# Optimization experiments

Measured on AMD Instinct MI355X. Metric: run time of the kernel, lower is better.

Reference implementation:

```python
import jax, jax.numpy as jnp
import numpy as np

N, E = 100000, 3200000
IN, HID, OUT, ED = 16, 64, 32, 3
BN_EPS = 1e-5


def setup_inputs() -> dict:
    key = jax.random.key(0)
    ks = jax.random.split(key, 40)
    d = {}
    d["x"] = jax.random.normal(ks[0], (N, IN), jnp.float32)
    d["edge_index"] = jax.random.randint(ks[1], (2, E), 0, N, dtype=jnp.int32)
    d["edge_attr"] = jax.random.normal(ks[2], (E, ED), jnp.float32)
    i = [3]
    def p(shape):
        w = jax.random.normal(ks[i[0]], shape, jnp.float32) * 0.05
        i[0] += 1
        return w
    for tag, nd in (("inj1", IN), ("inj2", HID), ("inj3", HID)):
        d[tag + "_w1"] = p((ED, nd)); d[tag + "_b1"] = p((nd,))
        d[tag + "_w2"] = p((nd, nd)); d[tag + "_b2"] = p((nd,))
    for tag, ci, co in (("conv1", IN, HID), ("conv2", HID, HID), ("conv3", HID, OUT)):
        d[tag + "_wl"] = p((ci, co)); d[tag + "_bl"] = p((co,))
        d[tag + "_wr"] = p((ci, co))
    for tag, c in (("bn1", HID), ("bn2", HID), ("bn3", OUT)):
        d[tag + "_w"] = p((c,)); d[tag + "_b"] = p((c,))
    return d


def _inject(x, src, dst, edge_attr, w1, b1, w2, b2):
    # edge MLP: [E, ED] -> [E, node_dim], sigmoid wind gate from column 2
    h = jax.nn.relu(edge_attr @ w1 + b1) @ w2 + b2
    gate = jax.nn.sigmoid(edge_attr[:, 2:3])
    msg = h * gate
    agg = jax.ops.segment_sum(msg, dst, num_segments=x.shape[0])
    return x + agg


def _sage(x, src, dst, wl, bl, wr):
    # PyG SAGEConv (mean aggr): lin_l(mean_{j in N(i)} x_j) + lin_r(x_i)
    n = x.shape[0]
    s = jax.ops.segment_sum(x[src], dst, num_segments=n)
    cnt = jax.ops.segment_sum(jnp.ones((src.shape[0], 1), x.dtype), dst, num_segments=n)
    mean = s / jnp.maximum(cnt, 1.0)
    return mean @ wl + bl + x @ wr


def _bn(x, w, b):
    # eval-mode BatchNorm with running_mean=0, running_var=1
    return x * (w / jnp.sqrt(1.0 + BN_EPS)) + b


def reference(x, edge_index, edge_attr,
              inj1_w1, inj1_b1, inj1_w2, inj1_b2,
              inj2_w1, inj2_b1, inj2_w2, inj2_b2,
              inj3_w1, inj3_b1, inj3_w2, inj3_b2,
              conv1_wl, conv1_bl, conv1_wr,
              conv2_wl, conv2_bl, conv2_wr,
              conv3_wl, conv3_bl, conv3_wr,
              bn1_w, bn1_b, bn2_w, bn2_b, bn3_w, bn3_b):
    src, dst = edge_index[0], edge_index[1]
    h = _inject(x, src, dst, edge_attr, inj1_w1, inj1_b1, inj1_w2, inj1_b2)
    h = jax.nn.relu(_bn(_sage(h, src, dst, conv1_wl, conv1_bl, conv1_wr), bn1_w, bn1_b))
    h = _inject(h, src, dst, edge_attr, inj2_w1, inj2_b1, inj2_w2, inj2_b2)
    h = jax.nn.relu(_bn(_sage(h, src, dst, conv2_wl, conv2_bl, conv2_wr), bn2_w, bn2_b))
    h = _inject(h, src, dst, edge_attr, inj3_w1, inj3_b1, inj3_w2, inj3_b2)
    h = jax.nn.relu(_bn(_sage(h, src, dst, conv3_wl, conv3_bl, conv3_wr), bn3_w, bn3_b))
    return h
```

## Files before the change

kernel.cpp:

```cpp
#include <hip/hip_runtime.h>
#include <math.h>

#define N_NODES 100000
#define N_EDGES 3200000
#define NB 391
#define CHUNK 4096
#define NCHUNK 782
#define HCHUNK 4096
#define NHCHUNK 782
#define CAPB 10240
#define NPW 4
#define NWAVES ((N_NODES + NPW - 1)/NPW)
#define NBLK_INJ ((NWAVES + 3)/4)

constexpr size_t al512(size_t x){ return (x + 511) & ~size_t(511); }
constexpr size_t o_bcnt = 0;
constexpr size_t o_bst  = al512(o_bcnt + 512*4);
constexpr size_t o_gb   = al512(o_bst  + 512*4);
constexpr size_t o_off  = al512(o_gb   + 512*4);
constexpr size_t o_srcp = al512(o_off  + ((size_t)N_NODES+1)*4);
constexpr size_t o_epk  = al512(o_srcp + (size_t)N_EDGES*4);
constexpr size_t o_U1   = al512(o_epk  + (size_t)N_EDGES*16);
constexpr size_t o_U2   = al512(o_U1   + (size_t)N_NODES*16*4);
constexpr size_t o_U3   = o_U2 + (size_t)N_NODES*64*4;
constexpr size_t o_gs   = al512(o_U3   + (size_t)N_NODES*64*4);
constexpr size_t o_h1   = al512(o_gs   + (size_t)N_NODES*4);
constexpr size_t o_m1   = al512(o_h1   + (size_t)N_NODES*16*4);
constexpr size_t o_rec  = o_U2;
constexpr size_t o_h2bf = o_epk;
constexpr size_t o_h3bf = o_epk + (size_t)N_NODES*128;
constexpr size_t o_m2   = o_U2;
constexpr size_t o_y3   = o_U1;
constexpr size_t o_m3p  = o_U2;

#define BN_RSQRT 0.9999950000374997f

__device__ __forceinline__ float4 ld4(const float* p){ return *(const float4*)p; }
__device__ __forceinline__ float fc(const float4& v, int i){ return ((const float*)&v)[i]; }
__device__ __forceinline__ float uf(unsigned u){ return __uint_as_float(u); }

typedef float v2f __attribute__((ext_vector_type(2)));
__device__ __forceinline__ v2f v2mk(float a, float b){ v2f v; v.x=a; v.y=b; return v; }
__device__ __forceinline__ v2f v2sp(float s){ v2f v; v.x=s; v.y=s; return v; }
__device__ __forceinline__ v2f v2fma(v2f a, v2f b, v2f c){ return __builtin_elementwise_fma(a,b,c); }
__device__ __forceinline__ v2f v2max0(v2f a){ return __builtin_elementwise_max(a, v2sp(0.f)); }

__device__ __forceinline__ unsigned f2bf(float x){
    unsigned u = __float_as_uint(x);
    u += 0x7fffu + ((u >> 16) & 1u);
    return u >> 16;
}

__global__ __launch_bounds__(256) void khistBin(const int* __restrict__ dst,
                                                int* __restrict__ binCnt){
    __shared__ int c[NB];
    int t = threadIdx.x;
    for(int i=t; i<NB; i+=256) c[i] = 0;
    __syncthreads();
    long base = (long)blockIdx.x*HCHUNK;
    int nrem = (int)(N_EDGES - base); if(nrem > HCHUNK) nrem = HCHUNK;
    for(int k=t; k<nrem; k+=256)
        atomicAdd(&c[dst[base+k] >> 8], 1);
    __syncthreads();
    for(int i=t; i<NB; i+=256)
        if(c[i]) atomicAdd(&binCnt[i], c[i]);
}

__global__ __launch_bounds__(512) void kscanBin(const int* __restrict__ binCnt,
                                                int* __restrict__ binStart,
                                                int* __restrict__ gbase){
    __shared__ int s[512];
    int t = threadIdx.x;
    int v = (t < NB) ? binCnt[t] : 0;
    s[t] = v; __syncthreads();
    for(int off=1; off<512; off<<=1){
        int a = (t>=off) ? s[t-off] : 0;
        __syncthreads(); s[t] += a; __syncthreads();
    }
    int ex = (t==0) ? 0 : s[t-1];
    if(t < NB){ binStart[t] = ex; gbase[t] = ex; }
    if(t == NB) binStart[NB] = s[NB-1];
}

__global__ __launch_bounds__(256) void kbinA(const int* __restrict__ src,
                                             const int* __restrict__ dst,
                                             const float* __restrict__ ea,
                                             int* __restrict__ gbase,
                                             unsigned* __restrict__ recD){
    __shared__ int cnt[NB], lofs[NB], gst[NB], lcnt[NB];
    __shared__ int sscan[256];
    __shared__ unsigned stage[CHUNK*3];
    __shared__ unsigned short binOf[CHUNK];
    int t = threadIdx.x;
    long e0i = (long)blockIdx.x*CHUNK;
    int nrem = (int)(N_EDGES - e0i); if(nrem > CHUNK) nrem = CHUNK;
    if(nrem <= 0) return;

    for(int b=t; b<NB; b+=256){ cnt[b]=0; lcnt[b]=0; }
    __syncthreads();
    for(int k=t; k<nrem; k+=256)
        atomicAdd(&cnt[dst[e0i+k] >> 8], 1);
    __syncthreads();
    int c0 = (2*t   < NB) ? cnt[2*t]   : 0;
    int c1 = (2*t+1 < NB) ? cnt[2*t+1] : 0;
    sscan[t] = c0 + c1;
    __syncthreads();
    for(int off=1; off<256; off<<=1){
        int v = (t>=off) ? sscan[t-off] : 0;
        __syncthreads(); sscan[t] += v; __syncthreads();
    }
    int base = (t==0) ? 0 : sscan[t-1];
    if(2*t   < NB) lofs[2*t]   = base;
    if(2*t+1 < NB) lofs[2*t+1] = base + c0;
    for(int b=t; b<NB; b+=256){
        int c = cnt[b];
        gst[b] = c ? atomicAdd(&gbase[b], c) : 0;
    }
    __syncthreads();
    for(int k=t; k<nrem; k+=256){
        long i = e0i + k;
        int d = dst[i];
        int s = src[i];
        float a0 = ea[i*3+0], a1 = ea[i*3+1], a2 = ea[i*3+2];
        int b = d >> 8;
        int p = lofs[b] + atomicAdd(&lcnt[b], 1);
        stage[3*p+0] = (unsigned)s | ((unsigned)(d & 255) << 17);
        stage[3*p+1] = (f2bf(a1)<<16) | f2bf(a0);
        stage[3*p+2] = __float_as_uint(a2);
        binOf[p] = (unsigned short)b;
    }
    __syncthreads();
    int total3 = nrem*3;
    for(int q=t; q<total3; q+=256){
        int p = q/3;
        int r = q - 3*p;
        int b = binOf[p];
        int g = gst[b] + (p - lofs[b]);
        recD[(size_t)3*g + r] = stage[q];
    }
}

__global__ __launch_bounds__(512) void kbinB(const unsigned* __restrict__ recD,
                                             const int* __restrict__ binStart,
                                             int* __restrict__ offs,
                                             int* __restrict__ srcp,
                                             float4* __restrict__ epk){
    __shared__ int pfx[257], lcnt[256];
    __shared__ int sscan[256];
    __shared__ unsigned short perm[CAPB];
    __shared__ unsigned char  nibOf[CAPB];
    int t = threadIdx.x;
    int b = blockIdx.x;
    int n0 = b*256;
    int nn = N_NODES - n0; if(nn > 256) nn = 256;
    int base = binStart[b];
    int m    = binStart[b+1] - base;
    for(int i=t; i<256; i+=512) lcnt[i] = 0;
    __syncthreads();
    for(int p=t; p<m; p+=512){
        unsigned w0 = recD[(size_t)3*(base+p)];
        int nib = (int)((w0 >> 17) & 255u);
        if(p < CAPB) nibOf[p] = (unsigned char)nib;
        atomicAdd(&lcnt[nib], 1);
    }
    __syncthreads();
    if(t < 256) sscan[t] = lcnt[t];
    __syncthreads();
    if(t < 256){
        for(int off=1; off<256; off<<=1){
            int v = (t>=off) ? sscan[t-off] : 0;
            __syncthreads(); sscan[t] += v; __syncthreads();
        }
        pfx[t+1] = sscan[t];
        if(t==0) pfx[0] = 0;
    } else {
        for(int off=1; off<256; off<<=1){ __syncthreads(); __syncthreads(); }
    }
    __syncthreads();
    for(int i=t; i<=nn; i+=512) offs[n0+i] = base + pfx[i];
    for(int i=t; i<256; i+=512) lcnt[i] = 0;
    __syncthreads();
    for(int p=t; p<m; p+=512){
        int nib = nibOf[p];
        int slot = pfx[nib] + atomicAdd(&lcnt[nib], 1);
        perm[slot] = (unsigned short)p;
    }
    __syncthreads();
    for(int s=t; s<m; s+=512){
        size_t q = (size_t)3*(base + (int)perm[s]);
        unsigned w0 = recD[q], w1 = recD[q+1], w2 = recD[q+2];
        float e2 = uf(w2);
        float gate = __builtin_amdgcn_rcpf(1.f + __expf(-e2));
        srcp[base+s] = (int)(w0 & 0x1FFFFu);
        epk [base+s] = make_float4(uf(w1<<16), uf(w1 & 0xffff0000u), e2, gate);
    }
}

#define ACC2(r) { \
    float h1_ = fmaf((r).z,wc1, fmaf((r).y,wb1, fmaf((r).x,wa1, bb1))); \
    a1 = fmaf(fmaxf(h1_,0.f), (r).w, a1); \
    v2f h2_ = v2fma(v2sp((r).z), wc2, v2fma(v2sp((r).y), wb2, v2fma(v2sp((r).x), wa2, bv2))); \
    a2 = v2fma(v2max0(h2_), v2sp((r).w), a2); \
    v2f h3_ = v2fma(v2sp((r).z), wc3, v2fma(v2sp((r).y), wb3, v2fma(v2sp((r).x), wa3, bv3))); \
    a3 = v2fma(v2max0(h3_), v2sp((r).w), a3); \
    g += (r).w; }

__global__ __launch_bounds__(256, 4) void kinject(const float4* __restrict__ epk, const int* __restrict__ offs,
                        const float* __restrict__ w11, const float* __restrict__ b11,
                        const float* __restrict__ w12, const float* __restrict__ b12,
                        const float* __restrict__ w13, const float* __restrict__ b13,
                        float* __restrict__ U1, float* __restrict__ U2,
                        float* __restrict__ U3, float* __restrict__ gsum){
    int wid = (blockIdx.x*256 + threadIdx.x) >> 6;
    int n0 = wid * NPW;
    if(n0 >= N_NODES) return;
    int n1 = n0 + NPW; if(n1 > N_NODES) n1 = N_NODES;
    int lane = threadIdx.x & 63;
    int half = lane >> 5, j = lane & 31, j16 = lane & 15;
    float wa1=w11[j16], wb1=w11[16+j16], wc1=w11[32+j16], bb1=b11[j16];
    v2f wa2=v2mk(w12[j],     w12[32+j]);
    v2f wb2=v2mk(w12[64+j],  w12[96+j]);
    v2f wc2=v2mk(w12[128+j], w12[160+j]);
    v2f bv2=v2mk(b12[j],     b12[32+j]);
    v2f wa3=v2mk(w13[j],     w13[32+j]);
    v2f wb3=v2mk(w13[64+j],  w13[96+j]);
    v2f wc3=v2mk(w13[128+j], w13[160+j]);
    v2f bv3=v2mk(b13[j],     b13[32+j]);

    int beg = offs[n0];
    for(int node=n0; node<n1; ++node){
        int end = offs[node+1];
        float a1=0.f, g=0.f;
        v2f a2=v2sp(0.f), a3=v2sp(0.f);
        int e = beg;
        int efull8 = beg + ((end - beg) & ~7);
        for(; e < efull8; e+=8){
            float4 r0 = epk[e + half];
            float4 r1 = epk[e + 2 + half];
            float4 r2 = epk[e + 4 + half];
            float4 r3 = epk[e + 6 + half];
            ACC2(r0);
            ACC2(r1);
            ACC2(r2);
            ACC2(r3);
        }
        for(; e < end; e+=4){
            int ee0 = e + half, ee1 = e + 2 + half;
            float4 r0 = (ee0 < end) ? epk[ee0] : make_float4(0.f,0.f,0.f,0.f);
            float4 r1 = (ee1 < end) ? epk[ee1] : make_float4(0.f,0.f,0.f,0.f);
            ACC2(r0);
            ACC2(r1);
        }
        a2.x += __shfl_xor(a2.x, 32); a2.y += __shfl_xor(a2.y, 32);
        a3.x += __shfl_xor(a3.x, 32); a3.y += __shfl_xor(a3.y, 32);
        a1   += __shfl_xor(a1, 16);   a1   += __shfl_xor(a1, 32);
        g    += __shfl_xor(g, 32);
        float v2_ = half ? a2.y : a2.x;
        float v3_ = half ? a3.y : a3.x;
        int col = j + 32*half;
        U2[(size_t)node*64 + col] = v2_;
        U3[(size_t)node*64 + col] = v3_;
        if(lane < 16) U1[node*16 + j16] = a1;
        if(lane == 0) gsum[node] = g;
        beg = end;
    }
}

__global__ void kgather16(const float* __restrict__ h, const int* __restrict__ srcp,
                          const int* __restrict__ offs, float* __restrict__ m){
    int gid = blockIdx.x*blockDim.x + threadIdx.x;
    int node = gid >> 6;
    if(node >= N_NODES) return;
    int lane = threadIdx.x & 63;
    int q = lane >> 4, d = lane & 15;
    int beg = offs[node], end = offs[node+1];
    float acc = 0.f;
    int e = beg + q;
    for(; e + 4 < end; e += 8){
        int s0 = srcp[e], s1 = srcp[e+4];
        float v0 = h[(size_t)s0*16 + d];
        float v1 = h[(size_t)s1*16 + d];
        acc += v0 + v1;
    }
    if(e < end) acc += h[(size_t)srcp[e]*16 + d];
    acc += __shfl_down(acc, 32);
    acc += __shfl_down(acc, 16);
    if(lane < 16){
        float c = fmaxf((float)(end-beg), 1.f);
        m[node*16 + lane] = acc / c;
    }
}

__global__ void kgather64bf(const unsigned* __restrict__ hbf, const int* __restrict__ srcp,
                            const int* __restrict__ offs, float* __restrict__ m){
    int gid = blockIdx.x*blockDim.x + threadIdx.x;
    int node = gid >> 6;
    if(node >= N_NODES) return;
    int lane = threadIdx.x & 63;
    int q = lane >> 4, j = lane & 15;
    int beg = offs[node], end = offs[node+1];
    float4 acc = make_float4(0.f,0.f,0.f,0.f);
    int e = beg;
    int efull16 = beg + ((end - beg) & ~15);
    for(; e < efull16; e+=16){
        int s0 = srcp[e + q],     s1 = srcp[e + 4 + q];
        int s2 = srcp[e + 8 + q], s3 = srcp[e + 12 + q];
        uint2 w0 = *(const uint2*)(hbf + (size_t)s0*32 + 2*j);
        uint2 w1 = *(const uint2*)(hbf + (size_t)s1*32 + 2*j);
        uint2 w2 = *(const uint2*)(hbf + (size_t)s2*32 + 2*j);
        uint2 w3 = *(const uint2*)(hbf + (size_t)s3*32 + 2*j);
        acc.x += uf(w0.x<<16); acc.y += uf(w0.x & 0xffff0000u);
        acc.z += uf(w0.y<<16); acc.w += uf(w0.y & 0xffff0000u);
        acc.x += uf(w1.x<<16); acc.y += uf(w1.x & 0xffff0000u);
        acc.z += uf(w1.y<<16); acc.w += uf(w1.y & 0xffff0000u);
        acc.x += uf(w2.x<<16); acc.y += uf(w2.x & 0xffff0000u);
        acc.z += uf(w2.y<<16); acc.w += uf(w2.y & 0xffff0000u);
        acc.x += uf(w3.x<<16); acc.y += uf(w3.x & 0xffff0000u);
        acc.z += uf(w3.y<<16); acc.w += uf(w3.y & 0xffff0000u);
    }
    int efull8 = beg + ((end - beg) & ~7);
    for(; e < efull8; e+=8){
        int s0 = srcp[e + q], s1 = srcp[e + 4 + q];
        uint2 w0 = *(const uint2*)(hbf + (size_t)s0*32 + 2*j);
        uint2 w1 = *(const uint2*)(hbf + (size_t)s1*32 + 2*j);
        acc.x += uf(w0.x<<16); acc.y += uf(w0.x & 0xffff0000u);
        acc.z += uf(w0.y<<16); acc.w += uf(w0.y & 0xffff0000u);
        acc.x += uf(w1.x<<16); acc.y += uf(w1.x & 0xffff0000u);
        acc.z += uf(w1.y<<16); acc.w += uf(w1.y & 0xffff0000u);
    }
    for(; e < end; e+=4){
        int ee = e + q;
        if(ee < end){
            int s = srcp[ee];
            uint2 w = *(const uint2*)(hbf + (size_t)s*32 + 2*j);
            acc.x += uf(w.x<<16); acc.y += uf(w.x & 0xffff0000u);
            acc.z += uf(w.y<<16); acc.w += uf(w.y & 0xffff0000u);
        }
    }
    acc.x += __shfl_xor(acc.x,16); acc.x += __shfl_xor(acc.x,32);
    acc.y += __shfl_xor(acc.y,16); acc.y += __shfl_xor(acc.y,32);
    acc.z += __shfl_xor(acc.z,16); acc.z += __shfl_xor(acc.z,32);
    acc.w += __shfl_xor(acc.w,16); acc.w += __shfl_xor(acc.w,32);
    if(lane < 16){
        float inv = 1.f / fmaxf((float)(end-beg), 1.f);
        float4 o; o.x=acc.x*inv; o.y=acc.y*inv; o.z=acc.z*inv; o.w=acc.w*inv;
        *(float4*)(m + (size_t)node*64 + 4*j) = o;
    }
}

__global__ void kgather32bf(const unsigned* __restrict__ y3, const int* __restrict__ srcp,
                            const int* __restrict__ offs, float* __restrict__ m){
    int gid = blockIdx.x*blockDim.x + threadIdx.x;
    int node = gid >> 6;
    if(node >= N_NODES) return;
    int lane = threadIdx.x & 63;
    int q = lane >> 4, j = lane & 15;
    int beg = offs[node], end = offs[node+1];
    float ax=0.f, ay=0.f;
    int e = beg;
    int efull = beg + ((end - beg) & ~7);
    for(; e < efull; e+=8){
        unsigned w0 = y3[(size_t)srcp[e + q]*16 + j];
        unsigned w1 = y3[(size_t)srcp[e + 4 + q]*16 + j];
        ax += uf(w0<<16); ay += uf(w0 & 0xffff0000u);
        ax += uf(w1<<16); ay += uf(w1 & 0xffff0000u);
    }
    for(; e < end; e+=4){
        int ee = e + q;
        if(ee < end){
            unsigned w = y3[(size_t)srcp[ee]*16 + j];
            ax += uf(w<<16); ay += uf(w & 0xffff0000u);
        }
    }
    ax += __shfl_xor(ax,16); ax += __shfl_xor(ax,32);
    ay += __shfl_xor(ay,16); ay += __shfl_xor(ay,32);
    if(lane < 16){
        float inv = 1.f / fmaxf((float)(end-beg), 1.f);
        float2 o; o.x = ax*inv; o.y = ay*inv;
        *(float2*)(m + (size_t)node*32 + 2*j) = o;
    }
}


__global__ __launch_bounds__(256) void kdense0(const float* __restrict__ x, const float* __restrict__ U1,
                        const float* __restrict__ gs, const float* __restrict__ w2,
                        const float* __restrict__ b2, float* __restrict__ h1){
    __shared__ float sw[256];
    int t = threadIdx.x;
    sw[t] = w2[t];
    __syncthreads();
    int idx = blockIdx.x*256 + t;
    int n = idx >> 4, j = idx & 15;
    float acc = x[idx] + gs[n]*b2[j];
    const float4* row = (const float4*)(U1 + n*16);
    #pragma unroll
    for(int i4=0;i4<4;i4++){
        float4 r = row[i4];
        acc += r.x*sw[(i4*4+0)*16 + j];
        acc += r.y*sw[(i4*4+1)*16 + j];
        acc += r.z*sw[(i4*4+2)*16 + j];
        acc += r.w*sw[(i4*4+3)*16 + j];
    }
    h1[idx] = acc;
}

__global__ __launch_bounds__(256) void kdense1(const float* __restrict__ m1, const float* __restrict__ h1,
                        const float* __restrict__ U2, const float* __restrict__ gs,
                        const float* __restrict__ wl, const float* __restrict__ bl,
                        const float* __restrict__ wr,
                        const float* __restrict__ w2, const float* __restrict__ b2,
                        const float* __restrict__ bnw, const float* __restrict__ bnb,
                        unsigned* __restrict__ h2bf){
    __shared__ float4 swl[16*16];
    __shared__ float4 swr[16*16];
    __shared__ float4 sw2[64*16];
    int t = threadIdx.x;
    swl[t] = ((const float4*)wl)[t];
    swr[t] = ((const float4*)wr)[t];
    #pragma unroll
    for(int k=0;k<4;k++) sw2[t + 256*k] = ((const float4*)w2)[t + 256*k];
    __syncthreads();

    int w = t>>6, l = t&63;
    int jg = l&15, j0 = jg*4, ng = l>>4;
    int nb = blockIdx.x*64 + w*16 + ng*4;
    int nn[4];
    #pragma unroll
    for(int k=0;k<4;k++) nn[k] = (nb+k < N_NODES) ? nb+k : N_NODES-1;

    float a[4][4], b[4][4];
    float4 blv = ld4(bl + j0);
    float4 b2v = ld4(b2 + j0);
    #pragma unroll
    for(int k=0;k<4;k++){
        float g = gs[nn[k]];
        a[k][0]=blv.x; a[k][1]=blv.y; a[k][2]=blv.z; a[k][3]=blv.w;
        b[k][0]=g*b2v.x; b[k][1]=g*b2v.y; b[k][2]=g*b2v.z; b[k][3]=g*b2v.w;
    }
    #pragma unroll
    for(int i=0;i<16;i+=4){
        float4 rm[4], rh[4];
        #pragma unroll
        for(int k=0;k<4;k++){ rm[k] = ld4(m1 + nn[k]*16 + i); rh[k] = ld4(h1 + nn[k]*16 + i); }
        #pragma unroll
        for(int ii=0;ii<4;ii++){
            float4 wL = swl[(i+ii)*16 + jg];
            float4 wR = swr[(i+ii)*16 + jg];
            #pragma unroll
            for(int k=0;k<4;k++){
                float vm = fc(rm[k],ii), vh = fc(rh[k],ii);
                a[k][0] = fmaf(vm,wL.x, fmaf(vh,wR.x, a[k][0]));
                a[k][1] = fmaf(vm,wL.y, fmaf(vh,wR.y, a[k][1]));
                a[k][2] = fmaf(vm,wL.z, fmaf(vh,wR.z, a[k][2]));
                a[k][3] = fmaf(vm,wL.w, fmaf(vh,wR.w, a[k][3]));
            }
        }
    }
    #pragma unroll 4
    for(int i=0;i<64;i+=4){
        float4 ru[4];
        #pragma unroll
        for(int k=0;k<4;k++) ru[k] = ld4(U2 + (size_t)nn[k]*64 + i);
        #pragma unroll
        for(int ii=0;ii<4;ii++){
            float4 wv = sw2[(i+ii)*16 + jg];
            #pragma unroll
            for(int k=0;k<4;k++){
                float vu = fc(ru[k],ii);
                b[k][0] = fmaf(vu,wv.x,b[k][0]);
                b[k][1] = fmaf(vu,wv.y,b[k][1]);
                b[k][2] = fmaf(vu,wv.z,b[k][2]);
                b[k][3] = fmaf(vu,wv.w,b[k][3]);
            }
        }
    }
    float4 bw = ld4(bnw + j0), bb = ld4(bnb + j0);
    #pragma unroll
    for(int k=0;k<4;k++){
        if(nb+k < N_NODES){
            float ox = fmaxf(a[k][0]*(bw.x*BN_RSQRT)+bb.x,0.f) + b[k][0];
            float oy = fmaxf(a[k][1]*(bw.y*BN_RSQRT)+bb.y,0.f) + b[k][1];
            float oz = fmaxf(a[k][2]*(bw.z*BN_RSQRT)+bb.z,0.f) + b[k][2];
            float ow = fmaxf(a[k][3]*(bw.w*BN_RSQRT)+bb.w,0.f) + b[k][3];
            uint2 pk; pk.x = f2bf(ox) | (f2bf(oy)<<16); pk.y = f2bf(oz) | (f2bf(ow)<<16);
            *(uint2*)(h2bf + (size_t)(nb+k)*32 + (j0>>1)) = pk;
        }
    }
}

__global__ __launch_bounds__(256) void kdense2(const float* __restrict__ m2, const unsigned* __restrict__ h2bf,
                        const float* __restrict__ U3, const float* __restrict__ gs,
                        const float* __restrict__ wl, const float* __restrict__ bl,
                        const float* __restrict__ wr,
                        const float* __restrict__ w2, const float* __restrict__ b2,
                        const float* __restrict__ bnw, const float* __restrict__ bnb,
                        const float* __restrict__ wl3,
                        unsigned* __restrict__ h3bf, unsigned* __restrict__ y3){
    __shared__ float4 swl[64*16];
    __shared__ float4 swr[64*16];
    __shared__ float4 sw2[64*16];
    __shared__ float4 swl3[64*8];
    __shared__ unsigned sh3[64*32];
    int t = threadIdx.x;
    #pragma unroll
    for(int k=0;k<4;k++){
        swl[t + 256*k] = ((const float4*)wl)[t + 256*k];
        swr[t + 256*k] = ((const float4*)wr)[t + 256*k];
        sw2[t + 256*k] = ((const float4*)w2)[t + 256*k];
    }
    swl3[t] = ((const float4*)wl3)[t];
    swl3[t+256] = ((const float4*)wl3)[t+256];
    __syncthreads();

    int w = t>>6, l = t&63;
    int jg = l&15, j0 = jg*4, ng = l>>4;
    int ln0 = w*16 + ng*4;
    int nb = blockIdx.x*64 + ln0;
    int nn[4];
    #pragma unroll
    for(int k=0;k<4;k++) nn[k] = (nb+k < N_NODES) ? nb+k : N_NODES-1;

    float a[4][4], b[4][4];
    float4 blv = ld4(bl + j0);
    float4 b2v = ld4(b2 + j0);
    #pragma unroll
    for(int k=0;k<4;k++){
        float g = gs[nn[k]];
        a[k][0]=blv.x; a[k][1]=blv.y; a[k][2]=blv.z; a[k][3]=blv.w;
        b[k][0]=g*b2v.x; b[k][1]=g*b2v.y; b[k][2]=g*b2v.z; b[k][3]=g*b2v.w;
    }
    #pragma unroll 4
    for(int i=0;i<64;i+=4){
        float4 rm[4], rh[4];
        #pragma unroll
        for(int k=0;k<4;k++){
            rm[k] = ld4(m2 + (size_t)nn[k]*64 + i);
            uint2 hw = *(const uint2*)(h2bf + (size_t)nn[k]*32 + (i>>1));
            rh[k].x = uf(hw.x<<16); rh[k].y = uf(hw.x & 0xffff0000u);
            rh[k].z = uf(hw.y<<16); rh[k].w = uf(hw.y & 0xffff0000u);
        }
        #pragma unroll
        for(int ii=0;ii<4;ii++){
            float4 wL = swl[(i+ii)*16 + jg];
            float4 wR = swr[(i+ii)*16 + jg];
            #pragma unroll
            for(int k=0;k<4;k++){
                float vm = fc(rm[k],ii), vh = fc(rh[k],ii);
                a[k][0] = fmaf(vm,wL.x, fmaf(vh,wR.x, a[k][0]));
                a[k][1] = fmaf(vm,wL.y, fmaf(vh,wR.y, a[k][1]));
                a[k][2] = fmaf(vm,wL.z, fmaf(vh,wR.z, a[k][2]));
                a[k][3] = fmaf(vm,wL.w, fmaf(vh,wR.w, a[k][3]));
            }
        }
    }
    #pragma unroll 4
    for(int i=0;i<64;i+=4){
        float4 ru[4];
        #pragma unroll
        for(int k=0;k<4;k++) ru[k] = ld4(U3 + (size_t)nn[k]*64 + i);
        #pragma unroll
        for(int ii=0;ii<4;ii++){
            float4 wv = sw2[(i+ii)*16 + jg];
            #pragma unroll
            for(int k=0;k<4;k++){
                float vu = fc(ru[k],ii);
                b[k][0] = fmaf(vu,wv.x,b[k][0]);
                b[k][1] = fmaf(vu,wv.y,b[k][1]);
                b[k][2] = fmaf(vu,wv.z,b[k][2]);
                b[k][3] = fmaf(vu,wv.w,b[k][3]);
            }
        }
    }
    float4 bw = ld4(bnw + j0), bb = ld4(bnb + j0);
    #pragma unroll
    for(int k=0;k<4;k++){
        float ox = fmaxf(a[k][0]*(bw.x*BN_RSQRT)+bb.x,0.f) + b[k][0];
        float oy = fmaxf(a[k][1]*(bw.y*BN_RSQRT)+bb.y,0.f) + b[k][1];
        float oz = fmaxf(a[k][2]*(bw.z*BN_RSQRT)+bb.z,0.f) + b[k][2];
        float ow = fmaxf(a[k][3]*(bw.w*BN_RSQRT)+bb.w,0.f) + b[k][3];
        uint2 pk; pk.x = f2bf(ox) | (f2bf(oy)<<16); pk.y = f2bf(oz) | (f2bf(ow)<<16);
        *(uint2*)(sh3 + (ln0+k)*32 + (j0>>1)) = pk;
        if(nb+k < N_NODES)
            *(uint2*)(h3bf + (size_t)(nb+k)*32 + (j0>>1)) = pk;
    }
    __syncthreads();
    int nl = t >> 2, jc = t & 3;
    int gnode = blockIdx.x*64 + nl;
    if(gnode < N_NODES){
        float y[8] = {0.f,0.f,0.f,0.f,0.f,0.f,0.f,0.f};
        #pragma unroll 8
        for(int i2=0; i2<32; ++i2){
            unsigned hw = sh3[nl*32 + i2];
            float h0 = uf(hw<<16), h1 = uf(hw & 0xffff0000u);
            float4 A0 = swl3[(2*i2)*8 + jc*2];
            float4 A1 = swl3[(2*i2)*8 + jc*2 + 1];
            float4 B0 = swl3[(2*i2+1)*8 + jc*2];
            float4 B1 = swl3[(2*i2+1)*8 + jc*2 + 1];
            y[0] = fmaf(h0,A0.x, fmaf(h1,B0.x, y[0]));
            y[1] = fmaf(h0,A0.y, fmaf(h1,B0.y, y[1]));
            y[2] = fmaf(h0,A0.z, fmaf(h1,B0.z, y[2]));
            y[3] = fmaf(h0,A0.w, fmaf(h1,B0.w, y[3]));
            y[4] = fmaf(h0,A1.x, fmaf(h1,B1.x, y[4]));
            y[5] = fmaf(h0,A1.y, fmaf(h1,B1.y, y[5]));
            y[6] = fmaf(h0,A1.z, fmaf(h1,B1.z, y[6]));
            y[7] = fmaf(h0,A1.w, fmaf(h1,B1.w, y[7]));
        }
        uint4 pk;
        pk.x = f2bf(y[0]) | (f2bf(y[1])<<16);
        pk.y = f2bf(y[2]) | (f2bf(y[3])<<16);
        pk.z = f2bf(y[4]) | (f2bf(y[5])<<16);
        pk.w = f2bf(y[6]) | (f2bf(y[7])<<16);
        *(uint4*)(y3 + (size_t)gnode*16 + jc*4) = pk;
    }
}

__global__ __launch_bounds__(256) void kdense3(const float* __restrict__ m3p, const unsigned* __restrict__ h3bf,
                        const float* __restrict__ bl,
                        const float* __restrict__ wr,
                        const float* __restrict__ bnw, const float* __restrict__ bnb,
                        float* __restrict__ out){
    __shared__ float4 swr[64*8];
    int t = threadIdx.x;
    #pragma unroll
    for(int k=0;k<2;k++) swr[t + 256*k] = ((const float4*)wr)[t + 256*k];
    __syncthreads();

    int w = t>>6, l = t&63;
    int jg = l&7, j0 = jg*4, ng = l>>3;
    int nb = blockIdx.x*128 + w*32 + ng*4;
    int nn[4];
    #pragma unroll
    for(int k=0;k<4;k++) nn[k] = (nb+k < N_NODES) ? nb+k : N_NODES-1;

    float a[4][4];
    float4 blv = ld4(bl + j0);
    #pragma unroll
    for(int k=0;k<4;k++){
        float4 mp = ld4(m3p + (size_t)nn[k]*32 + j0);
        a[k][0]=blv.x+mp.x; a[k][1]=blv.y+mp.y; a[k][2]=blv.z+mp.z; a[k][3]=blv.w+mp.w;
    }
    #pragma unroll 4
    for(int i=0;i<64;i+=4){
        float4 rh[4];
        #pragma unroll
        for(int k=0;k<4;k++){
            uint2 hw = *(const uint2*)(h3bf + (size_t)nn[k]*32 + (i>>1));
            rh[k].x = uf(hw.x<<16); rh[k].y = uf(hw.x & 0xffff0000u);
            rh[k].z = uf(hw.y<<16); rh[k].w = uf(hw.y & 0xffff0000u);
        }
        #pragma unroll
        for(int ii=0;ii<4;ii++){
            float4 wR = swr[(i+ii)*8 + jg];
            #pragma unroll
            for(int k=0;k<4;k++){
                float vh = fc(rh[k],ii);
                a[k][0] = fmaf(vh,wR.x,a[k][0]);
                a[k][1] = fmaf(vh,wR.y,a[k][1]);
                a[k][2] = fmaf(vh,wR.z,a[k][2]);
                a[k][3] = fmaf(vh,wR.w,a[k][3]);
            }
        }
    }
    float4 bw = ld4(bnw + j0), bb = ld4(bnb + j0);
    #pragma unroll
    for(int k=0;k<4;k++){
        if(nb+k < N_NODES){
            float4 o;
            o.x = fmaxf(a[k][0]*(bw.x*BN_RSQRT)+bb.x,0.f);
            o.y = fmaxf(a[k][1]*(bw.y*BN_RSQRT)+bb.y,0.f);
            o.z = fmaxf(a[k][2]*(bw.z*BN_RSQRT)+bb.z,0.f);
            o.w = fmaxf(a[k][3]*(bw.w*BN_RSQRT)+bb.w,0.f);
            *(float4*)(out + (size_t)(nb+k)*32 + j0) = o;
        }
    }
}

extern "C" void kernel_launch(void* const* d_in, const int* in_sizes, int n_in,
                              void* d_out, int out_size, void* d_ws, size_t ws_size,
                              hipStream_t stream){
    const float* x    = (const float*)d_in[0];
    const int*   ei   = (const int*)  d_in[1];
    const float* ea   = (const float*)d_in[2];
    const float* i1w1 = (const float*)d_in[3];
    const float* i1b1 = (const float*)d_in[4];
    const float* i1w2 = (const float*)d_in[5];
    const float* i1b2 = (const float*)d_in[6];
    const float* i2w1 = (const float*)d_in[7];
    const float* i2b1 = (const float*)d_in[8];
    const float* i2w2 = (const float*)d_in[9];
    const float* i2b2 = (const float*)d_in[10];
    const float* i3w1 = (const float*)d_in[11];
    const float* i3b1 = (const float*)d_in[12];
    const float* i3w2 = (const float*)d_in[13];
    const float* i3b2 = (const float*)d_in[14];
    const float* c1wl = (const float*)d_in[15];
    const float* c1bl = (const float*)d_in[16];
    const float* c1wr = (const float*)d_in[17];
    const float* c2wl = (const float*)d_in[18];
    const float* c2bl = (const float*)d_in[19];
    const float* c2wr = (const float*)d_in[20];
    const float* c3wl = (const float*)d_in[21];
    const float* c3bl = (const float*)d_in[22];
    const float* c3wr = (const float*)d_in[23];
    const float* bn1w = (const float*)d_in[24];
    const float* bn1b = (const float*)d_in[25];
    const float* bn2w = (const float*)d_in[26];
    const float* bn2b = (const float*)d_in[27];
    const float* bn3w = (const float*)d_in[28];
    const float* bn3b = (const float*)d_in[29];

    char* ws = (char*)d_ws;
    int*      bcnt = (int*)     (ws + o_bcnt);
    int*      bst  = (int*)     (ws + o_bst);
    int*      gb   = (int*)     (ws + o_gb);
    int*      offs = (int*)     (ws + o_off);
    int*      srcp = (int*)     (ws + o_srcp);
    float4*   epk  = (float4*)  (ws + o_epk);
    unsigned* recD = (unsigned*)(ws + o_rec);
    float*    U1   = (float*)   (ws + o_U1);
    float*    U2   = (float*)   (ws + o_U2);
    float*    U3   = (float*)   (ws + o_U3);
    float*    gs   = (float*)   (ws + o_gs);
    float*    h1   = (float*)   (ws + o_h1);
    float*    m1   = (float*)   (ws + o_m1);
    unsigned* h2bf = (unsigned*)(ws + o_h2bf);
    unsigned* h3bf = (unsigned*)(ws + o_h3bf);
    float*    m2   = (float*)   (ws + o_m2);
    unsigned* y3   = (unsigned*)(ws + o_y3);
    float*    m3p  = (float*)   (ws + o_m3p);

    const int* src = ei;
    const int* dst = ei + N_EDGES;

    hipMemsetAsync(bcnt, 0, 512*4, stream);
    khistBin <<<NHCHUNK, 256, 0, stream>>>(dst, bcnt);
    kscanBin <<<1,       512, 0, stream>>>(bcnt, bst, gb);
    kbinA  <<<NCHUNK, 256, 0, stream>>>(src, dst, ea, gb, recD);
    kbinB  <<<NB,     512, 0, stream>>>(recD, bst, offs, srcp, epk);

    kinject <<<NBLK_INJ, 256, 0, stream>>>(epk, offs,
                                           i1w1, i1b1, i2w1, i2b1, i3w1, i3b1,
                                           U1, U2, U3, gs);
    kdense0 <<<N_NODES*16/256, 256, 0, stream>>>(x, U1, gs, i1w2, i1b2, h1);
    kgather16<<<N_NODES/4, 256, 0, stream>>>(h1, srcp, offs, m1);
    kdense1 <<<(N_NODES+63)/64, 256, 0, stream>>>(m1, h1, U2, gs,
                                                 c1wl, c1bl, c1wr, i2w2, i2b2,
                                                 bn1w, bn1b, h2bf);
    kgather64bf<<<N_NODES/4, 256, 0, stream>>>(h2bf, srcp, offs, m2);
    kdense2 <<<(N_NODES+63)/64, 256, 0, stream>>>(m2, h2bf, U3, gs,
                                                 c2wl, c2bl, c2wr, i3w2, i3b2,
                                                 bn2w, bn2b, c3wl, h3bf, y3);
    kgather32bf<<<N_NODES/4, 256, 0, stream>>>(y3, srcp, offs, m3p);
    kdense3 <<<(N_NODES+127)/128, 256, 0, stream>>>(m3p, h3bf, c3bl, c3wr,
                                                 bn3w, bn3b, (float*)d_out);
}
```

Measured before the change: 653.7 us.

## Stage edge records into LDS with double-buffered async loads in kinject

```diff
diff --git a/kernel.cpp b/kernel.cpp
--- a/kernel.cpp
+++ b/kernel.cpp
@@ -9,7 +9,7 @@
 #define HCHUNK 4096
 #define NHCHUNK 782
 #define CAPB 10240
-#define NPW 4
+#define NPW 2
 #define NWAVES ((N_NODES + NPW - 1)/NPW)
 #define NBLK_INJ ((NWAVES + 3)/4)
 
@@ -51,6 +51,14 @@
     return u >> 16;
 }
 
+__device__ __forceinline__ void glds16(const void* g, void* l){
+    __builtin_amdgcn_global_load_lds(
+        (const __attribute__((address_space(1))) void*)g,
+        (__attribute__((address_space(3)))       void*)l,
+        16, 0, 0);
+}
+#define WAITVM(n) { asm volatile("s_waitcnt vmcnt(" #n ")" ::: "memory"); __builtin_amdgcn_sched_barrier(0); }
+
 __global__ __launch_bounds__(256) void khistBin(const int* __restrict__ dst,
                                                 int* __restrict__ binCnt){
     __shared__ int c[NB];
@@ -205,17 +213,31 @@
     a3 = v2fma(v2max0(h3_), v2sp((r).w), a3); \
     g += (r).w; }
 
-__global__ __launch_bounds__(256, 4) void kinject(const float4* __restrict__ epk, const int* __restrict__ offs,
+#define FLUSH(nd) { \
+    float f2x=a2.x, f2y=a2.y, f3x=a3.x, f3y=a3.y, f1=a1, fg=g; \
+    f2x += __shfl_xor(f2x,32); f2y += __shfl_xor(f2y,32); \
+    f3x += __shfl_xor(f3x,32); f3y += __shfl_xor(f3y,32); \
+    f1  += __shfl_xor(f1,16);  f1  += __shfl_xor(f1,32); \
+    fg  += __shfl_xor(fg,32); \
+    int col = j + 32*half; \
+    U2[(size_t)(nd)*64 + col] = half ? f2y : f2x; \
+    U3[(size_t)(nd)*64 + col] = half ? f3y : f3x; \
+    if(lane < 16) U1[(size_t)(nd)*16 + j16] = f1; \
+    if(lane == 0) gsum[nd] = fg; }
+
+__global__ __launch_bounds__(256) void kinject(const float4* __restrict__ epk, const int* __restrict__ offs,
                         const float* __restrict__ w11, const float* __restrict__ b11,
                         const float* __restrict__ w12, const float* __restrict__ b12,
                         const float* __restrict__ w13, const float* __restrict__ b13,
                         float* __restrict__ U1, float* __restrict__ U2,
                         float* __restrict__ U3, float* __restrict__ gsum){
-    int wid = (blockIdx.x*256 + threadIdx.x) >> 6;
+    __shared__ float4 stagebuf[4][2][64];
+    int tid = threadIdx.x;
+    int wslot = tid >> 6;
+    int wid = (blockIdx.x*256 + tid) >> 6;
     int n0 = wid * NPW;
     if(n0 >= N_NODES) return;
-    int n1 = n0 + NPW; if(n1 > N_NODES) n1 = N_NODES;
-    int lane = threadIdx.x & 63;
+    int lane = tid & 63;
     int half = lane >> 5, j = lane & 31, j16 = lane & 15;
     float wa1=w11[j16], wb1=w11[16+j16], wc1=w11[32+j16], bb1=b11[j16];
     v2f wa2=v2mk(w12[j],     w12[32+j]);
@@ -227,43 +249,63 @@
     v2f wc3=v2mk(w13[128+j], w13[160+j]);
     v2f bv3=v2mk(b13[j],     b13[32+j]);
 
-    int beg = offs[n0];
-    for(int node=n0; node<n1; ++node){
-        int end = offs[node+1];
-        float a1=0.f, g=0.f;
-        v2f a2=v2sp(0.f), a3=v2sp(0.f);
-        int e = beg;
-        int efull8 = beg + ((end - beg) & ~7);
-        for(; e < efull8; e+=8){
-            float4 r0 = epk[e + half];
-            float4 r1 = epk[e + 2 + half];
-            float4 r2 = epk[e + 4 + half];
-            float4 r3 = epk[e + 6 + half];
-            ACC2(r0);
-            ACC2(r1);
-            ACC2(r2);
-            ACC2(r3);
-        }
-        for(; e < end; e+=4){
-            int ee0 = e + half, ee1 = e + 2 + half;
-            float4 r0 = (ee0 < end) ? epk[ee0] : make_float4(0.f,0.f,0.f,0.f);
-            float4 r1 = (ee1 < end) ? epk[ee1] : make_float4(0.f,0.f,0.f,0.f);
-            ACC2(r0);
-            ACC2(r1);
-        }
-        a2.x += __shfl_xor(a2.x, 32); a2.y += __shfl_xor(a2.y, 32);
-        a3.x += __shfl_xor(a3.x, 32); a3.y += __shfl_xor(a3.y, 32);
-        a1   += __shfl_xor(a1, 16);   a1   += __shfl_xor(a1, 32);
-        g    += __shfl_xor(g, 32);
-        float v2_ = half ? a2.y : a2.x;
-        float v3_ = half ? a3.y : a3.x;
-        int col = j + 32*half;
-        U2[(size_t)node*64 + col] = v2_;
-        U3[(size_t)node*64 + col] = v3_;
-        if(lane < 16) U1[node*16 + j16] = a1;
-        if(lane == 0) gsum[node] = g;
-        beg = end;
-    }
+    int b0 = offs[n0];
+    int e0n = offs[n0+1];
+    int b1 = e0n;
+    int e1n = offs[n0+2];
+
+    int ca = (e0n - b0 + 63) >> 6;
+    int cb = (e1n - b1 + 63) >> 6;
+    int T  = ca + cb;
+
+    float4* buf0 = stagebuf[wslot][0];
+    float4* buf1 = stagebuf[wslot][1];
+    const char* base = (const char*)epk;
+
+    float a1=0.f, g=0.f;
+    v2f a2=v2sp(0.f), a3=v2sp(0.f);
+
+    if(ca == 0) FLUSH(n0);
+
+    if(T > 0){
+        {
+            int s0 = (0 < ca) ? b0 : b1;
+            int ee = (0 < ca) ? e0n : e1n;
+            long srci = (long)(s0 + lane);
+            long cl   = (long)(ee - 1);
+            if(srci > cl) srci = cl;
+            glds16(base + srci*16, buf0);
+        }
+        for(int t=0; t<T; ++t){
+            if(t+1 < T){
+                int tn = t+1;
+                int s0 = (tn < ca) ? b0 + (tn<<6) : b1 + ((tn-ca)<<6);
+                int ee = (tn < ca) ? e0n : e1n;
+                long srci = (long)(s0 + lane);
+                long cl   = (long)(ee - 1);
+                if(srci > cl) srci = cl;
+                glds16(base + srci*16, (tn&1) ? buf1 : buf0);
+                WAITVM(1);
+            } else {
+                WAITVM(0);
+            }
+            float4* cur = (t&1) ? buf1 : buf0;
+            int s0 = (t < ca) ? b0 + (t<<6) : b1 + ((t-ca)<<6);
+            int ee = (t < ca) ? e0n : e1n;
+            int lim = ee - s0; if(lim > 64) lim = 64;
+            if(lim == 64){
+                #pragma unroll 8
+                for(int k=0;k<32;k++){ float4 r = cur[2*k+half]; ACC2(r); }
+            } else {
+                for(int k=half; k<lim; k+=2){ float4 r = cur[k]; ACC2(r); }
+            }
+            if(t == ca-1){
+                FLUSH(n0);
+                a1=0.f; g=0.f; a2=v2sp(0.f); a3=v2sp(0.f);
+            }
+        }
+    }
+    FLUSH(n0+1);
 }
 
 __global__ void kgather16(const float* __restrict__ h, const int* __restrict__ srcp,
```

New measurement: 653.1 us. No clear change (-0.1%).
